# Kernel optimization log

Hardware: AMD Instinct MI355X
Metric: run time of the kernel (lower is better)

Reference implementation:

```python
import jax, jax.numpy as jnp
import numpy as np
import math

B, S, HID, H = 8, 512, 768, 12
D = HID // H  # 64
LABEL_VOCAB = 2 * 40 + 1  # 81
EPS = 1e-5


def layernorm(x, g, b):
    mu = jnp.mean(x, axis=-1, keepdims=True)
    var = jnp.var(x, axis=-1, keepdims=True)
    return (x - mu) * jax.lax.rsqrt(var + EPS) * g + b


def setup_inputs() -> dict:
    key = jax.random.key(0)
    ks = jax.random.split(key, 12)
    s = 0.02
    return {
        "hidden_states": jax.random.normal(ks[0], (B, S, HID), jnp.float32),
        "attention_mask": jnp.zeros((B, 1, 1, S), jnp.float32),
        "graph_arc": jax.random.randint(ks[1], (B, S, S), 0, LABEL_VOCAB, jnp.int32),
        "Wq": jax.random.normal(ks[2], (HID, HID), jnp.float32) * s,
        "bq": jnp.zeros((HID,), jnp.float32),
        "Wk": jax.random.normal(ks[3], (HID, HID), jnp.float32) * s,
        "bk": jnp.zeros((HID,), jnp.float32),
        "Wv": jax.random.normal(ks[4], (HID, HID), jnp.float32) * s,
        "bv": jnp.zeros((HID,), jnp.float32),
        "rel_k": jax.random.normal(ks[5], (LABEL_VOCAB, D), jnp.float32) * s,
        "rel_v": jax.random.normal(ks[6], (LABEL_VOCAB, D), jnp.float32) * s,
        "ln_k_g": jnp.ones((D,), jnp.float32),
        "ln_k_b": jnp.zeros((D,), jnp.float32),
        "ln_v_g": jnp.ones((D,), jnp.float32),
        "ln_v_b": jnp.zeros((D,), jnp.float32),
    }


def reference(hidden_states, attention_mask, graph_arc, Wq, bq, Wk, bk, Wv, bv,
              rel_k, rel_v, ln_k_g, ln_k_b, ln_v_g, ln_v_b):
    # projections -> [B, H, S, D]
    def split_heads(x):
        return x.reshape(B, S, H, D).transpose(0, 2, 1, 3)

    q = split_heads(hidden_states @ Wq + bq)
    k = split_heads(hidden_states @ Wk + bk)
    v = split_heads(hidden_states @ Wv + bv)

    # relation embeddings [B, S, S, D], layernormed over D
    dp_keys = layernorm(rel_k[graph_arc], ln_k_g, ln_k_b)
    dp_values = layernorm(rel_v[graph_arc], ln_v_g, ln_v_b)

    scores = jnp.einsum('bhqd,bhkd->bhqk', q, k) / math.sqrt(D)
    # relative_matmul_dp: per (b, q-position) GEMM of q[B,S,H,D] with dp_keys^T
    scores = scores + jnp.einsum('bqhd,bqkd->bhqk', q.transpose(0, 2, 1, 3), dp_keys)
    scores = scores + attention_mask

    probs = jax.nn.softmax(scores, axis=-1)  # dropout p=0 (eval)

    ctx = jnp.einsum('bhqk,bhkd->bqhd', probs, v)
    # relative_matmul_dpv
    ctx = ctx + jnp.einsum('bhqk,bqkd->bqhd', probs, dp_values)
    return ctx.reshape(B, S, HID)
```

## Files before the change

kernel.cpp:

```cpp
#include <hip/hip_runtime.h>
#include <hip/hip_bf16.h>

#define BB 8
#define SS 512
#define HIDV 768
#define HH 12
#define DD 64
#define LV 81

typedef __attribute__((ext_vector_type(8))) short short8v;
typedef __attribute__((ext_vector_type(4))) short short4v;
typedef __attribute__((ext_vector_type(4))) float f32x4;

#define MFMA16(a, b, c) __builtin_amdgcn_mfma_f32_16x16x32_bf16(a, b, c, 0, 0, 0)

__device__ __forceinline__ short f2bf(float f) {
    __hip_bfloat16 h = __float2bfloat16(f);
    return *reinterpret_cast<short*>(&h);
}
__device__ __forceinline__ void gload16(const void* g, void* l) {
    __builtin_amdgcn_global_load_lds((const __attribute__((address_space(1))) void*)g,
                                     (__attribute__((address_space(3))) void*)l, 16, 0, 0);
}

__global__ __launch_bounds__(256) void prep_ln_kernel(
    const float* __restrict__ rel_k, const float* __restrict__ rel_v,
    const float* __restrict__ gk, const float* __restrict__ bk,
    const float* __restrict__ gv, const float* __restrict__ bv,
    short* __restrict__ lnkb, short* __restrict__ lnvT) {
    __shared__ float ln_lds[2 * LV][DD];
    int t = threadIdx.x;
    if (t < 2 * LV) {
        bool isv = (t >= LV);
        int r = isv ? t - LV : t;
        const float* row = (isv ? rel_v : rel_k) + r * DD;
        const float* g = isv ? gv : gk;
        const float* be = isv ? bv : bk;
        float mu = 0.f;
        for (int d = 0; d < DD; ++d) mu += row[d];
        mu *= (1.f / DD);
        float var = 0.f;
        for (int d = 0; d < DD; ++d) { float x = row[d] - mu; var += x * x; }
        var *= (1.f / DD);
        float rs = rsqrtf(var + 1e-5f);
        for (int d = 0; d < DD; ++d) ln_lds[t][d] = (row[d] - mu) * rs * g[d] + be[d];
    }
    __syncthreads();
    for (int i = t; i < 96 * DD; i += 256) {
        int l = i >> 6, d = i & 63;
        lnkb[i] = (l < LV) ? f2bf(ln_lds[l][d]) : (short)0;
    }
    for (int i = t; i < DD * 96; i += 256) {
        int d = i / 96, ll = i - d * 96;
        lnvT[i] = (ll < LV) ? f2bf(ln_lds[LV + ll][d]) : (short)0;
    }
}

__global__ __launch_bounds__(256) void conv_hidden_kernel(const float* __restrict__ in,
                                                          short* __restrict__ out) {
    int i = (blockIdx.x * 256 + threadIdx.x) * 4;
    float4 v = *reinterpret_cast<const float4*>(&in[i]);
    short4v o; o[0] = f2bf(v.x); o[1] = f2bf(v.y); o[2] = f2bf(v.z); o[3] = f2bf(v.w);
    *reinterpret_cast<short4v*>(&out[i]) = o;
}

__global__ __launch_bounds__(256) void transw_kernel(
    const float* __restrict__ Wq, const float* __restrict__ Wk, const float* __restrict__ Wv,
    short* __restrict__ WqT, short* __restrict__ WkT, short* __restrict__ WvT) {
    const float* W; short* O;
    if (blockIdx.z == 0) { W = Wq; O = WqT; }
    else if (blockIdx.z == 1) { W = Wk; O = WkT; }
    else { W = Wv; O = WvT; }
    __shared__ float tile[32][33];
    int k0 = blockIdx.y * 32, n0 = blockIdx.x * 32;
    int t = threadIdx.x;
    int r = t >> 3, c4 = (t & 7) * 4;
    float4 v = *reinterpret_cast<const float4*>(&W[(size_t)(k0 + r) * HIDV + n0 + c4]);
    tile[r][c4 + 0] = v.x; tile[r][c4 + 1] = v.y; tile[r][c4 + 2] = v.z; tile[r][c4 + 3] = v.w;
    __syncthreads();
    short4v o;
    o[0] = f2bf(tile[c4 + 0][r]); o[1] = f2bf(tile[c4 + 1][r]);
    o[2] = f2bf(tile[c4 + 2][r]); o[3] = f2bf(tile[c4 + 3][r]);
    *reinterpret_cast<short4v*>(&O[(size_t)(n0 + r) * HIDV + k0 + c4]) = o;
}

__global__ __launch_bounds__(256) void arcpack_kernel(const int* __restrict__ arc,
                                                      unsigned int* __restrict__ arcP) {
    __shared__ unsigned int tbuf[64][129];
    const int tid = threadIdx.x;
    const int b = blockIdx.y;
    const int q0 = blockIdx.x * 64;
    for (int i = tid; i < 64 * 128; i += 256) {
        int r = i >> 7, c4 = i & 127;
        int4 v = *reinterpret_cast<const int4*>(&arc[((size_t)(b * SS) + q0 + r) * SS + 4 * c4]);
        tbuf[r][c4] = (unsigned)(v.x & 255) | ((unsigned)(v.y & 255) << 8) |
                      ((unsigned)(v.z & 255) << 16) | ((unsigned)(v.w & 255) << 24);
    }
    __syncthreads();
    for (int i = tid; i < 128 * 64; i += 256) {
        int k4 = i >> 6, r = i & 63;
        arcP[((size_t)b * 128 + k4) * SS + q0 + r] = tbuf[r][k4];
    }
}

__global__ __launch_bounds__(256) void qkv_gemm_kernel(
    const short* __restrict__ Abf,
    const short* __restrict__ WqT, const short* __restrict__ WkT, const short* __restrict__ WvT,
    const float* __restrict__ bq, const float* __restrict__ bk, const float* __restrict__ bv,
    short* __restrict__ qo, short* __restrict__ ko, short* __restrict__ vto) {
    const short* Bt; const float* bias;
    int z = blockIdx.z;
    if (z == 0) { Bt = WqT; bias = bq; }
    else if (z == 1) { Bt = WkT; bias = bk; }
    else { Bt = WvT; bias = bv; }

    __shared__ short smem[8192];
    short* As = smem;
    short* Bs = smem + 4096;

    const int tid = threadIdx.x;
    const int lane = tid & 63, w = tid >> 6;
    const int li = lane & 15, g = lane >> 4;
    const int wr = w >> 1, wc = w & 1;
    const int m0 = blockIdx.y * 64, n0 = blockIdx.x * 64;

    f32x4 acc[2][2];
    for (int ra = 0; ra < 2; ++ra)
        for (int cb = 0; cb < 2; ++cb)
            for (int r = 0; r < 4; ++r) acc[ra][cb][r] = 0.f;

#pragma unroll 1
    for (int k0 = 0; k0 < HIDV; k0 += 64) {
#pragma unroll
        for (int j = 0; j < 2; ++j) {
            int c = j * 256 + tid;
            int row = c >> 3, s = c & 7;
            int src = s ^ (row & 7);
            gload16(Abf + (size_t)(m0 + row) * HIDV + k0 + src * 8, As + c * 8);
            gload16(Bt + (size_t)(n0 + row) * HIDV + k0 + src * 8, Bs + c * 8);
        }
        __syncthreads();
#pragma unroll
        for (int c = 0; c < 2; ++c) {
            short8v af[2], bf[2];
#pragma unroll
            for (int ra = 0; ra < 2; ++ra) {
                int row = 32 * wr + 16 * ra + li;
                int chunk = (4 * c + g) ^ (row & 7);
                af[ra] = *reinterpret_cast<const short8v*>(&As[row * 64 + chunk * 8]);
            }
#pragma unroll
            for (int cb = 0; cb < 2; ++cb) {
                int rowb = 32 * wc + 16 * cb + li;
                int chunk = (4 * c + g) ^ (rowb & 7);
                bf[cb] = *reinterpret_cast<const short8v*>(&Bs[rowb * 64 + chunk * 8]);
            }
#pragma unroll
            for (int ra = 0; ra < 2; ++ra)
#pragma unroll
                for (int cb = 0; cb < 2; ++cb)
                    acc[ra][cb] = MFMA16(af[ra], bf[cb], acc[ra][cb]);
        }
        __syncthreads();
    }

    const int h = n0 >> 6;
    const int bidx = m0 >> 9;
    if (z < 2) {
        short* dst = (z == 0) ? qo : ko;
        float sc = (z == 0) ? 1.f : 0.125f;
#pragma unroll
        for (int ra = 0; ra < 2; ++ra)
#pragma unroll
            for (int cb = 0; cb < 2; ++cb) {
                int n = 32 * wc + 16 * cb + li;
                float bv_ = bias[n0 + n];
#pragma unroll
                for (int r = 0; r < 4; ++r) {
                    int m = m0 + 32 * wr + 16 * ra + 4 * g + r;
                    int s = m & 511;
                    dst[(((size_t)bidx * HH + h) * SS + s) * DD + n] =
                        f2bf((acc[ra][cb][r] + bv_) * sc);
                }
            }
    } else {
        short* Cs = smem;
#pragma unroll
        for (int ra = 0; ra < 2; ++ra)
#pragma unroll
            for (int cb = 0; cb < 2; ++cb) {
                int nl = 32 * wc + 16 * cb + li;
                float bv_ = bias[n0 + nl];
#pragma unroll
                for (int r = 0; r < 4; ++r) {
                    int ml = 32 * wr + 16 * ra + 4 * g + r;
                    Cs[nl * 72 + ml] = f2bf(acc[ra][cb][r] + bv_);
                }
            }
        __syncthreads();
        for (int c = tid; c < 512; c += 256) {
            int dl = c >> 3, s8 = (c & 7) * 8;
            short8v vv = *reinterpret_cast<const short8v*>(&Cs[dl * 72 + s8]);
            *reinterpret_cast<short8v*>(
                &vto[(((size_t)bidx * HH + h) * DD + dl) * SS + (m0 & 511) + s8]) = vv;
        }
    }
}

__global__ __launch_bounds__(256, 2) void attn_kernel(
    const short* __restrict__ qb, const short* __restrict__ kb, const short* __restrict__ vt,
    const unsigned int* __restrict__ arcP, const float* __restrict__ maskp,
    const short* __restrict__ lnkb, const short* __restrict__ lnvT,
    float* __restrict__ outp) {
    __shared__ float qlds[4][16][84];
    __shared__ float bucket[4][16][100];

    const int tid = threadIdx.x;
    const int w = tid >> 6, lane = tid & 63;
    const int li = lane & 15, g = lane >> 4;
    const int bx = blockIdx.x;
    const int b = bx & 7;
    const int rest = bx >> 3;
    const int h = rest % HH, qt = rest / HH;
    const int bh = b * HH + h;
    const int q0 = qt * 64 + w * 16;

    const short* kbp = kb + (size_t)bh * SS * DD;
    const short* vbp = vt + (size_t)bh * DD * SS;
    const unsigned int* apb = arcP + (size_t)b * 128 * SS;
    const float* mkb = maskp + (size_t)b * SS;

    for (int i = lane; i < 16 * 100; i += 64) (&bucket[w][0][0])[i] = 0.f;

    short8v qf0, qf1;
    {
        const short* qrow = qb + ((size_t)bh * SS + q0 + li) * DD + 8 * g;
        qf0 = *reinterpret_cast<const short8v*>(qrow);
        qf1 = *reinterpret_cast<const short8v*>(qrow + 32);
    }

#pragma unroll
    for (int ct = 0; ct < 6; ++ct) {
        f32x4 a = {0.f, 0.f, 0.f, 0.f};
        short8v b0 = *reinterpret_cast<const short8v*>(&lnkb[(16 * ct + li) * DD + 8 * g]);
        short8v b1 = *reinterpret_cast<const short8v*>(&lnkb[(16 * ct + li) * DD + 32 + 8 * g]);
        a = MFMA16(qf0, b0, a);
        a = MFMA16(qf1, b1, a);
        if (16 * ct + li < 84)
#pragma unroll
            for (int r = 0; r < 4; ++r) qlds[w][4 * g + r][16 * ct + li] = a[r];
    }

    f32x4 oacc[4];
    for (int t = 0; t < 4; ++t) for (int r = 0; r < 4; ++r) oacc[t][r] = 0.f;

    short8v kf[8];
    unsigned int a_[2][4];
    float4 m_[2][4];
    float qv_[2][16];
#pragma unroll
    for (int t = 0; t < 4; ++t) {
        const short* kr = kbp + (size_t)(16 * t + li) * DD + 8 * g;
        kf[2 * t] = *reinterpret_cast<const short8v*>(kr);
        kf[2 * t + 1] = *reinterpret_cast<const short8v*>(kr + 32);
        a_[0][t] = apb[(size_t)(4 * t + g) * SS + q0 + li];
        m_[0][t] = *reinterpret_cast<const float4*>(&mkb[16 * t + 4 * g]);
    }
#pragma unroll
    for (int t = 0; t < 4; ++t) {
        const unsigned int a4 = a_[0][t];
        qv_[0][4 * t + 0] = qlds[w][li][a4 & 255];
        qv_[0][4 * t + 1] = qlds[w][li][(a4 >> 8) & 255];
        qv_[0][4 * t + 2] = qlds[w][li][(a4 >> 16) & 255];
        qv_[0][4 * t + 3] = qlds[w][li][a4 >> 24];
    }

#pragma unroll
    for (int kt = 0; kt < 8; ++kt) {
        const int cur = kt & 1, nxt = cur ^ 1;
        const int kb0 = kt * 64;

        f32x4 sacc[4];
#pragma unroll
        for (int t = 0; t < 4; ++t) {
            f32x4 a = {0.f, 0.f, 0.f, 0.f};
            a = MFMA16(kf[2 * t], qf0, a);
            a = MFMA16(kf[2 * t + 1], qf1, a);
            sacc[t] = a;
        }

        if (kt < 7) {
#pragma unroll
            for (int t = 0; t < 4; ++t) {
                const short* kr = kbp + (size_t)(kb0 + 64 + 16 * t + li) * DD + 8 * g;
                kf[2 * t] = *reinterpret_cast<const short8v*>(kr);
                kf[2 * t + 1] = *reinterpret_cast<const short8v*>(kr + 32);
                a_[nxt][t] = apb[(size_t)((kt + 1) * 16 + 4 * t + g) * SS + q0 + li];
                m_[nxt][t] = *reinterpret_cast<const float4*>(&mkb[kb0 + 64 + 16 * t + 4 * g]);
            }
#pragma unroll
            for (int t = 0; t < 4; ++t) {
                const unsigned int a4 = a_[nxt][t];
                qv_[nxt][4 * t + 0] = qlds[w][li][a4 & 255];
                qv_[nxt][4 * t + 1] = qlds[w][li][(a4 >> 8) & 255];
                qv_[nxt][4 * t + 2] = qlds[w][li][(a4 >> 16) & 255];
                qv_[nxt][4 * t + 3] = qlds[w][li][a4 >> 24];
            }
        }

        float p[16];
#pragma unroll
        for (int t = 0; t < 4; ++t) {
            p[4 * t + 0] = __expf(sacc[t][0] + qv_[cur][4 * t + 0] + m_[cur][t].x);
            p[4 * t + 1] = __expf(sacc[t][1] + qv_[cur][4 * t + 1] + m_[cur][t].y);
            p[4 * t + 2] = __expf(sacc[t][2] + qv_[cur][4 * t + 2] + m_[cur][t].z);
            p[4 * t + 3] = __expf(sacc[t][3] + qv_[cur][4 * t + 3] + m_[cur][t].w);
        }

#pragma unroll
        for (int t = 0; t < 4; ++t) {
            const unsigned int a4 = a_[cur][t];
            unsafeAtomicAdd(&bucket[w][li][a4 & 255], p[4 * t + 0]);
            unsafeAtomicAdd(&bucket[w][li][(a4 >> 8) & 255], p[4 * t + 1]);
            unsafeAtomicAdd(&bucket[w][li][(a4 >> 16) & 255], p[4 * t + 2]);
            unsafeAtomicAdd(&bucket[w][li][a4 >> 24], p[4 * t + 3]);
        }

        short8v pfrag[2];
#pragma unroll
        for (int t = 0; t < 4; ++t)
#pragma unroll
            for (int r = 0; r < 4; ++r) pfrag[t >> 1][4 * (t & 1) + r] = f2bf(p[4 * t + r]);
#pragma unroll
        for (int dt = 0; dt < 2; ++dt) {
#pragma unroll
            for (int t2 = 0; t2 < 4; ++t2) {
                const short* vr = vbp + (size_t)(16 * t2 + li) * SS + kb0 + 32 * dt + 4 * g;
                short4v v0 = *reinterpret_cast<const short4v*>(vr);
                short4v v1 = *reinterpret_cast<const short4v*>(vr + 16);
                short8v vf;
                vf[0] = v0[0]; vf[1] = v0[1]; vf[2] = v0[2]; vf[3] = v0[3];
                vf[4] = v1[0]; vf[5] = v1[1]; vf[6] = v1[2]; vf[7] = v1[3];
                oacc[t2] = MFMA16(pfrag[dt], vf, oacc[t2]);
            }
        }
    }

    float lsum = 0.f;
#pragma unroll
    for (int j = 0; j < 24; ++j) {
        int c = 24 * g + j;
        lsum += (c < 81) ? bucket[w][li][c] : 0.f;
    }
    lsum += __shfl_xor(lsum, 16);
    lsum += __shfl_xor(lsum, 32);
    float inv = 1.f / lsum;
    float invr[4];
#pragma unroll
    for (int r = 0; r < 4; ++r) invr[r] = __shfl(inv, 4 * g + r);

    f32x4 racc[4];
    for (int t = 0; t < 4; ++t) for (int r = 0; r < 4; ++r) racc[t][r] = 0.f;
#pragma unroll
    for (int c = 0; c < 3; ++c) {
        f32x4 b0 = *reinterpret_cast<const f32x4*>(&bucket[w][li][8 * g + 32 * c]);
        f32x4 b1 = *reinterpret_cast<const f32x4*>(&bucket[w][li][8 * g + 32 * c + 4]);
        short8v bfr;
        bfr[0] = f2bf(b0[0]); bfr[1] = f2bf(b0[1]); bfr[2] = f2bf(b0[2]); bfr[3] = f2bf(b0[3]);
        bfr[4] = f2bf(b1[0]); bfr[5] = f2bf(b1[1]); bfr[6] = f2bf(b1[2]); bfr[7] = f2bf(b1[3]);
#pragma unroll
        for (int t2 = 0; t2 < 4; ++t2) {
            short8v lf = *reinterpret_cast<const short8v*>(
                &lnvT[(16 * t2 + li) * 96 + 8 * g + 32 * c]);
            racc[t2] = MFMA16(bfr, lf, racc[t2]);
        }
    }

#pragma unroll
    for (int t2 = 0; t2 < 4; ++t2)
#pragma unroll
        for (int r = 0; r < 4; ++r) {
            int row = q0 + 4 * g + r;
            outp[((size_t)b * SS + row) * HIDV + h * DD + 16 * t2 + li] =
                (oacc[t2][r] + racc[t2][r]) * invr[r];
        }
}

extern "C" void kernel_launch(void* const* d_in, const int* in_sizes, int n_in,
                              void* d_out, int out_size, void* d_ws, size_t ws_size,
                              hipStream_t stream) {
    const float* hidden = (const float*)d_in[0];
    const float* mask   = (const float*)d_in[1];
    const int*   arc    = (const int*)d_in[2];
    const float* Wq = (const float*)d_in[3];
    const float* bq = (const float*)d_in[4];
    const float* Wk = (const float*)d_in[5];
    const float* bk = (const float*)d_in[6];
    const float* Wv = (const float*)d_in[7];
    const float* bv = (const float*)d_in[8];
    const float* rel_k = (const float*)d_in[9];
    const float* rel_v = (const float*)d_in[10];
    const float* lng_k = (const float*)d_in[11];
    const float* lnb_k = (const float*)d_in[12];
    const float* lng_v = (const float*)d_in[13];
    const float* lnb_v = (const float*)d_in[14];
    float* out = (float*)d_out;

    char* p = (char*)d_ws;
    auto carve = [&](size_t bytes) { char* r = p; p += (bytes + 255) & ~(size_t)255; return r; };
    short* lnkb = (short*)carve((size_t)96 * DD * 2);
    short* lnvT = (short*)carve((size_t)DD * 96 * 2);
    short* hbf  = (short*)carve((size_t)BB * SS * HIDV * 2);
    short* WqT  = (short*)carve((size_t)HIDV * HIDV * 2);
    short* WkT  = (short*)carve((size_t)HIDV * HIDV * 2);
    short* WvT  = (short*)carve((size_t)HIDV * HIDV * 2);
    const size_t per = (size_t)BB * HH * SS * DD;
    short* qbuf = (short*)carve(per * 2);
    short* kbuf = (short*)carve(per * 2);
    short* vtb  = (short*)carve(per * 2);
    unsigned int* arcP = (unsigned int*)carve((size_t)BB * 128 * SS * 4);

    prep_ln_kernel<<<1, 256, 0, stream>>>(rel_k, rel_v, lng_k, lnb_k, lng_v, lnb_v, lnkb, lnvT);
    conv_hidden_kernel<<<(BB * SS * HIDV) / 1024, 256, 0, stream>>>(hidden, hbf);
    transw_kernel<<<dim3(24, 24, 3), 256, 0, stream>>>(Wq, Wk, Wv, WqT, WkT, WvT);
    arcpack_kernel<<<dim3(8, BB), 256, 0, stream>>>(arc, arcP);
    qkv_gemm_kernel<<<dim3(HIDV / 64, (BB * SS) / 64, 3), 256, 0, stream>>>(
        hbf, WqT, WkT, WvT, bq, bk, bv, qbuf, kbuf, vtb);
    attn_kernel<<<dim3(BB * HH * 8), 256, 0, stream>>>(
        qbuf, kbuf, vtb, arcP, mask, lnkb, lnvT, out);
}
```

Baseline: 196.0 us.

## Fuse prep kernels into one launch and prefetch V fragments early in attention

Merges the hidden-state bf16 conversion, weight transpose and arc packing kernels into a single launch that branches on block index. The layernorm prep kernel now writes bf16 outputs directly and drops its shared staging buffer. In the attention loop, V fragments are loaded into registers right after the score MFMAs so their latency overlaps the softmax and bucket work. This removes launch overhead and gaps between kernels, at the cost of more register pressure in the attention kernel and a larger shared-memory allocation for every fused prep block.

Result: faster. 192.1 us (-2.0%).

```diff
diff --git a/kernel.cpp b/kernel.cpp
--- a/kernel.cpp
+++ b/kernel.cpp
@@ -28,78 +28,87 @@
     const float* __restrict__ gk, const float* __restrict__ bk,
     const float* __restrict__ gv, const float* __restrict__ bv,
     short* __restrict__ lnkb, short* __restrict__ lnvT) {
-    __shared__ float ln_lds[2 * LV][DD];
     int t = threadIdx.x;
-    if (t < 2 * LV) {
-        bool isv = (t >= LV);
-        int r = isv ? t - LV : t;
-        const float* row = (isv ? rel_v : rel_k) + r * DD;
-        const float* g = isv ? gv : gk;
-        const float* be = isv ? bv : bk;
-        float mu = 0.f;
-        for (int d = 0; d < DD; ++d) mu += row[d];
-        mu *= (1.f / DD);
-        float var = 0.f;
-        for (int d = 0; d < DD; ++d) { float x = row[d] - mu; var += x * x; }
-        var *= (1.f / DD);
-        float rs = rsqrtf(var + 1e-5f);
-        for (int d = 0; d < DD; ++d) ln_lds[t][d] = (row[d] - mu) * rs * g[d] + be[d];
-    }
-    __syncthreads();
-    for (int i = t; i < 96 * DD; i += 256) {
-        int l = i >> 6, d = i & 63;
-        lnkb[i] = (l < LV) ? f2bf(ln_lds[l][d]) : (short)0;
-    }
-    for (int i = t; i < DD * 96; i += 256) {
-        int d = i / 96, ll = i - d * 96;
-        lnvT[i] = (ll < LV) ? f2bf(ln_lds[LV + ll][d]) : (short)0;
-    }
-}
-
-__global__ __launch_bounds__(256) void conv_hidden_kernel(const float* __restrict__ in,
-                                                          short* __restrict__ out) {
-    int i = (blockIdx.x * 256 + threadIdx.x) * 4;
-    float4 v = *reinterpret_cast<const float4*>(&in[i]);
-    short4v o; o[0] = f2bf(v.x); o[1] = f2bf(v.y); o[2] = f2bf(v.z); o[3] = f2bf(v.w);
-    *reinterpret_cast<short4v*>(&out[i]) = o;
-}
-
-__global__ __launch_bounds__(256) void transw_kernel(
+    if (t < 192) {
+        bool isv = (t >= 96);
+        int r = isv ? t - 96 : t;
+        if (r < LV) {
+            const float* row = (isv ? rel_v : rel_k) + r * DD;
+            const float* g = isv ? gv : gk;
+            const float* be = isv ? bv : bk;
+            float mu = 0.f;
+            for (int d = 0; d < DD; ++d) mu += row[d];
+            mu *= (1.f / DD);
+            float var = 0.f;
+            for (int d = 0; d < DD; ++d) { float x = row[d] - mu; var += x * x; }
+            var *= (1.f / DD);
+            float rs = rsqrtf(var + 1e-5f);
+            if (!isv) {
+                for (int d = 0; d < DD; ++d)
+                    lnkb[r * DD + d] = f2bf((row[d] - mu) * rs * g[d] + be[d]);
+            } else {
+                for (int d = 0; d < DD; ++d)
+                    lnvT[d * 96 + r] = f2bf((row[d] - mu) * rs * g[d] + be[d]);
+            }
+        } else {
+            if (!isv) for (int d = 0; d < DD; ++d) lnkb[r * DD + d] = 0;
+            else      for (int d = 0; d < DD; ++d) lnvT[d * 96 + r] = 0;
+        }
+    }
+}
+
+#define NCONV 3072
+#define NTRANS 1728
+#define NARC 64
+__global__ __launch_bounds__(256) void prep_fused_kernel(
+    const float* __restrict__ hidden, short* __restrict__ hbf,
     const float* __restrict__ Wq, const float* __restrict__ Wk, const float* __restrict__ Wv,
-    short* __restrict__ WqT, short* __restrict__ WkT, short* __restrict__ WvT) {
-    const float* W; short* O;
-    if (blockIdx.z == 0) { W = Wq; O = WqT; }
-    else if (blockIdx.z == 1) { W = Wk; O = WkT; }
-    else { W = Wv; O = WvT; }
-    __shared__ float tile[32][33];
-    int k0 = blockIdx.y * 32, n0 = blockIdx.x * 32;
-    int t = threadIdx.x;
-    int r = t >> 3, c4 = (t & 7) * 4;
-    float4 v = *reinterpret_cast<const float4*>(&W[(size_t)(k0 + r) * HIDV + n0 + c4]);
-    tile[r][c4 + 0] = v.x; tile[r][c4 + 1] = v.y; tile[r][c4 + 2] = v.z; tile[r][c4 + 3] = v.w;
-    __syncthreads();
-    short4v o;
-    o[0] = f2bf(tile[c4 + 0][r]); o[1] = f2bf(tile[c4 + 1][r]);
-    o[2] = f2bf(tile[c4 + 2][r]); o[3] = f2bf(tile[c4 + 3][r]);
-    *reinterpret_cast<short4v*>(&O[(size_t)(n0 + r) * HIDV + k0 + c4]) = o;
-}
-
-__global__ __launch_bounds__(256) void arcpack_kernel(const int* __restrict__ arc,
-                                                      unsigned int* __restrict__ arcP) {
-    __shared__ unsigned int tbuf[64][129];
+    short* __restrict__ WqT, short* __restrict__ WkT, short* __restrict__ WvT,
+    const int* __restrict__ arc, unsigned int* __restrict__ arcP) {
+    __shared__ unsigned int sbuf[64 * 129];
+    const int bid = blockIdx.x;
     const int tid = threadIdx.x;
-    const int b = blockIdx.y;
-    const int q0 = blockIdx.x * 64;
-    for (int i = tid; i < 64 * 128; i += 256) {
-        int r = i >> 7, c4 = i & 127;
-        int4 v = *reinterpret_cast<const int4*>(&arc[((size_t)(b * SS) + q0 + r) * SS + 4 * c4]);
-        tbuf[r][c4] = (unsigned)(v.x & 255) | ((unsigned)(v.y & 255) << 8) |
-                      ((unsigned)(v.z & 255) << 16) | ((unsigned)(v.w & 255) << 24);
-    }
-    __syncthreads();
-    for (int i = tid; i < 128 * 64; i += 256) {
-        int k4 = i >> 6, r = i & 63;
-        arcP[((size_t)b * 128 + k4) * SS + q0 + r] = tbuf[r][k4];
+
+    if (bid < NCONV) {
+        int i = (bid * 256 + tid) * 4;
+        float4 v = *reinterpret_cast<const float4*>(&hidden[i]);
+        short4v o; o[0] = f2bf(v.x); o[1] = f2bf(v.y); o[2] = f2bf(v.z); o[3] = f2bf(v.w);
+        *reinterpret_cast<short4v*>(&hbf[i]) = o;
+    } else if (bid < NCONV + NTRANS) {
+        int e = bid - NCONV;
+        int z = e / 576, rem = e - z * 576;
+        int by = rem / 24, bxx = rem - by * 24;
+        const float* W; short* O;
+        if (z == 0) { W = Wq; O = WqT; }
+        else if (z == 1) { W = Wk; O = WkT; }
+        else { W = Wv; O = WvT; }
+        float* tile = reinterpret_cast<float*>(sbuf);
+        int k0 = by * 32, n0 = bxx * 32;
+        int r = tid >> 3, c4 = (tid & 7) * 4;
+        float4 v = *reinterpret_cast<const float4*>(&W[(size_t)(k0 + r) * HIDV + n0 + c4]);
+        tile[r * 33 + c4 + 0] = v.x; tile[r * 33 + c4 + 1] = v.y;
+        tile[r * 33 + c4 + 2] = v.z; tile[r * 33 + c4 + 3] = v.w;
+        __syncthreads();
+        short4v o;
+        o[0] = f2bf(tile[(c4 + 0) * 33 + r]); o[1] = f2bf(tile[(c4 + 1) * 33 + r]);
+        o[2] = f2bf(tile[(c4 + 2) * 33 + r]); o[3] = f2bf(tile[(c4 + 3) * 33 + r]);
+        *reinterpret_cast<short4v*>(&O[(size_t)(n0 + r) * HIDV + k0 + c4]) = o;
+    } else {
+        int e = bid - NCONV - NTRANS;
+        int b = e >> 3, q0 = (e & 7) * 64;
+        unsigned int* tbuf = sbuf;
+        for (int i = tid; i < 64 * 128; i += 256) {
+            int r = i >> 7, c4 = i & 127;
+            int4 v = *reinterpret_cast<const int4*>(
+                &arc[((size_t)(b * SS) + q0 + r) * SS + 4 * c4]);
+            tbuf[r * 129 + c4] = (unsigned)(v.x & 255) | ((unsigned)(v.y & 255) << 8) |
+                                 ((unsigned)(v.z & 255) << 16) | ((unsigned)(v.w & 255) << 24);
+        }
+        __syncthreads();
+        for (int i = tid; i < 128 * 64; i += 256) {
+            int k4 = i >> 6, r = i & 63;
+            arcP[((size_t)b * 128 + k4) * SS + q0 + r] = tbuf[r * 129 + k4];
+        }
     }
 }
 
@@ -255,6 +264,7 @@
     for (int t = 0; t < 4; ++t) for (int r = 0; r < 4; ++r) oacc[t][r] = 0.f;
 
     short8v kf[8];
+    short4v vreg[16];
     unsigned int a_[2][4];
     float4 m_[2][4];
     float qv_[2][16];
@@ -289,6 +299,14 @@
             sacc[t] = a;
         }
 
+#pragma unroll
+        for (int dt = 0; dt < 2; ++dt)
+#pragma unroll
+            for (int t2 = 0; t2 < 4; ++t2) {
+                const short* vr = vbp + (size_t)(16 * t2 + li) * SS + kb0 + 32 * dt + 4 * g;
+                vreg[8 * dt + 2 * t2 + 0] = *reinterpret_cast<const short4v*>(vr);
+                vreg[8 * dt + 2 * t2 + 1] = *reinterpret_cast<const short4v*>(vr + 16);
+            }
         if (kt < 7) {
 #pragma unroll
             for (int t = 0; t < 4; ++t) {
@@ -335,9 +353,8 @@
         for (int dt = 0; dt < 2; ++dt) {
 #pragma unroll
             for (int t2 = 0; t2 < 4; ++t2) {
-                const short* vr = vbp + (size_t)(16 * t2 + li) * SS + kb0 + 32 * dt + 4 * g;
-                short4v v0 = *reinterpret_cast<const short4v*>(vr);
-                short4v v1 = *reinterpret_cast<const short4v*>(vr + 16);
+                short4v v0 = vreg[8 * dt + 2 * t2 + 0];
+                short4v v1 = vreg[8 * dt + 2 * t2 + 1];
                 short8v vf;
                 vf[0] = v0[0]; vf[1] = v0[1]; vf[2] = v0[2]; vf[3] = v0[3];
                 vf[4] = v1[0]; vf[5] = v1[1]; vf[6] = v1[2]; vf[7] = v1[3];
@@ -421,9 +438,8 @@
     unsigned int* arcP = (unsigned int*)carve((size_t)BB * 128 * SS * 4);
 
     prep_ln_kernel<<<1, 256, 0, stream>>>(rel_k, rel_v, lng_k, lnb_k, lng_v, lnb_v, lnkb, lnvT);
-    conv_hidden_kernel<<<(BB * SS * HIDV) / 1024, 256, 0, stream>>>(hidden, hbf);
-    transw_kernel<<<dim3(24, 24, 3), 256, 0, stream>>>(Wq, Wk, Wv, WqT, WkT, WvT);
-    arcpack_kernel<<<dim3(8, BB), 256, 0, stream>>>(arc, arcP);
+    prep_fused_kernel<<<dim3(NCONV + NTRANS + NARC), 256, 0, stream>>>(
+        hidden, hbf, Wq, Wk, Wv, WqT, WkT, WvT, arc, arcP);
     qkv_gemm_kernel<<<dim3(HIDV / 64, (BB * SS) / 64, 3), 256, 0, stream>>>(
         hbf, WqT, WkT, WvT, bq, bk, bv, qbuf, kbuf, vtb);
     attn_kernel<<<dim3(BB * HH * 8), 256, 0, stream>>>(
```
